# Optimization experiments

Measured on AMD Instinct MI355X. Metric: run time of the kernel, lower is better.

Reference implementation:

```python
import jax, jax.numpy as jnp
import numpy as np

B = 2          # number of point clouds (equal-size so the per-batch loop vmaps)
NB = 10000     # points per cloud
C_IN = 64
K = 16
BN_EPS = 1e-5

# grid_size_options: [tower, background, line]; line grid axis-2 is *5 per the source
GRID_T = jnp.array([0.1, 0.1, 0.1], dtype=jnp.float32)
GRID_B = jnp.array([1.0, 1.0, 1.0], dtype=jnp.float32)
GRID_L = jnp.array([0.3, 0.3, 0.3 * 5.0], dtype=jnp.float32)


def setup_inputs() -> dict:
    key = jax.random.key(0)
    ks = jax.random.split(key, 8)
    feat = jax.random.normal(ks[0], (B * NB, C_IN), dtype=jnp.float32)
    coord = jax.random.normal(ks[1], (B * NB, 3), dtype=jnp.float32) * 10.0
    batch = jnp.repeat(jnp.arange(B, dtype=jnp.int32), NB)
    # feature_judge params: Linear(C,32) -> BatchNorm1d(32) (inference mode) -> ReLU -> Linear(32,3)
    W1 = jax.random.normal(ks[2], (C_IN, 32), dtype=jnp.float32) * (1.0 / np.sqrt(C_IN))
    b1 = jnp.zeros((32,), dtype=jnp.float32)
    gamma = jnp.ones((32,), dtype=jnp.float32)
    beta = jnp.zeros((32,), dtype=jnp.float32)
    rmean = jnp.zeros((32,), dtype=jnp.float32)
    rvar = jnp.ones((32,), dtype=jnp.float32)
    W2 = jax.random.normal(ks[3], (32, 3), dtype=jnp.float32) * (1.0 / np.sqrt(32))
    b2 = jnp.zeros((3,), dtype=jnp.float32)
    return {"feat": feat, "coord": coord, "batch": batch,
            "W1": W1, "b1": b1, "gamma": gamma, "beta": beta,
            "rmean": rmean, "rvar": rvar, "W2": W2, "b2": b2}


def _per_batch(cb, fb, W1, b1, gamma, beta, rmean, rvar, W2, b2):
    # cb: [NB,3] coords, fb: [NB,C] feats
    nb = cb.shape[0]
    # brute-force Euclidean cdist, self-distance excluded (set to inf)
    sq = jnp.sum(cb * cb, axis=-1)                       # [NB]
    d2 = sq[:, None] + sq[None, :] - 2.0 * (cb @ cb.T)   # [NB,NB]
    d2 = jnp.maximum(d2, 0.0)
    diag = jnp.arange(nb)
    d2 = d2.at[diag, diag].set(jnp.inf)
    dist = jnp.sqrt(d2)
    # K nearest neighbors (smallest distances)
    neg_d, idx = jax.lax.top_k(-dist, K)                 # [NB,K]
    min_dist = -neg_d
    # local PCA: eigenvalues of 3x3 covariance == singular values (cov is SPD)
    neigh = cb[idx]                                      # [NB,K,3]
    centered = neigh - neigh.mean(axis=1, keepdims=True)
    cov = jnp.einsum('nkd,nke->nde', centered, centered) / (K - 1)
    S = jnp.linalg.eigvalsh(cov)[:, ::-1]                # descending, == svd singular values
    S_norm = S / (S.sum(axis=1, keepdims=True) + 1e-6)
    linearity = (S_norm[:, 0] - (S_norm[:, 1] + S_norm[:, 2]))[:, None]  # [NB,1]
    mean_dist = min_dist.mean(axis=1, keepdims=True)
    density = 1.0 / (mean_dist + 1e-6)
    # feature_judge MLP (BatchNorm in inference mode with running stats)
    h = fb @ W1 + b1
    h = (h - rmean) / jnp.sqrt(rvar + BN_EPS) * gamma + beta
    h = jax.nn.relu(h)
    logits = h @ W2 + b2
    probs = jax.nn.softmax(logits, axis=1)               # [NB,3]
    tower_prob = (density * 2.0 + probs[:, 0:1]) / 3.0
    background_prob = (jnp.maximum(1.0 - linearity, 1.0 - density) + probs[:, 1:2]) / 3.0
    line_prob = (linearity * 2.0 + probs[:, 2:3]) / 3.0
    grids = tower_prob * GRID_T + background_prob * GRID_B + line_prob * GRID_L + 1e-6
    return grids                                          # [NB,3]


def reference(feat, coord, batch, W1, b1, gamma, beta, rmean, rvar, W2, b2):
    # equal-size batches: the per-batch python loop becomes a vmap
    coord_b = coord.reshape(B, NB, 3)
    feat_b = feat.reshape(B, NB, C_IN)
    out = jax.vmap(lambda c, f: _per_batch(c, f, W1, b1, gamma, beta, rmean, rvar, W2, b2))(coord_b, feat_b)
    return out.reshape(B * NB, 3)
```

## Files before the change

kernel.cpp:

```cpp
#include <hip/hip_runtime.h>
#include <math.h>

#define NBP   10000
#define NBATCH 2
#define KNN   16
#define QT    16
#define PH    16
#define TILE  1250
#define NTHREADS 256
#define COLL  32

__global__ __launch_bounds__(NTHREADS)
void pfas_kernel(const float* __restrict__ feat,
                 const float* __restrict__ coord,
                 const float* __restrict__ W1,
                 const float* __restrict__ b1,
                 const float* __restrict__ gmm,
                 const float* __restrict__ bta,
                 const float* __restrict__ rmean,
                 const float* __restrict__ rvar,
                 const float* __restrict__ W2,
                 const float* __restrict__ b2,
                 float* __restrict__ out)
{
    __shared__ float4 s_cand[TILE];
    __shared__ float  s_tau[QT];
    __shared__ float2 s_coll[QT][COLL];
    __shared__ int    s_cnt[QT];

    const int tid = threadIdx.x;
    const int ql  = tid >> 4;
    const int ph  = tid & 15;
    const int b   = blockIdx.y;
    const int qi  = blockIdx.x * QT + ql;
    const int gq  = b * NBP + qi;

    const float qx = coord[3*gq], qy = coord[3*gq+1], qz = coord[3*gq+2];
    const float qsq = __fadd_rn(__fadd_rn(__fmul_rn(qx,qx), __fmul_rn(qy,qy)), __fmul_rn(qz,qz));

    if (tid < QT) s_cnt[tid] = 0;

    float td[KNN];
    #pragma unroll
    for (int s = 0; s < KNN; ++s) td[s] = INFINITY;

    for (int t0 = 0; t0 < NBP; t0 += TILE) {
        __syncthreads();
        for (int c = tid; c < TILE; c += NTHREADS) {
            const float* cp = coord + (size_t)(b*NBP + t0 + c) * 3;
            float x = cp[0], y = cp[1], z = cp[2];
            float sq = __fadd_rn(__fadd_rn(__fmul_rn(x,x), __fmul_rn(y,y)), __fmul_rn(z,z));
            s_cand[c] = make_float4(x, y, z, sq);
        }
        __syncthreads();
        for (int k = ph; k < TILE; k += PH) {
            const float4 c = s_cand[k];
            float dot = __fadd_rn(__fadd_rn(__fmul_rn(qx,c.x), __fmul_rn(qy,c.y)), __fmul_rn(qz,c.z));
            float d2  = __fsub_rn(__fadd_rn(qsq, c.w), __fmul_rn(2.0f, dot));
            float v = (t0 + k == qi) ? INFINITY : d2;
            #pragma unroll
            for (int s = 0; s < KNN; ++s) {
                float t = td[s];
                td[s] = fminf(t, v);
                v     = fmaxf(t, v);
            }
        }
    }

    __syncthreads();
    float* lists = reinterpret_cast<float*>(s_cand);
    #pragma unroll
    for (int s = 0; s < KNN; ++s) lists[s*NTHREADS + tid] = td[s];
    __syncthreads();

    if (tid < QT) {
        const int lane0 = tid * PH;
        int h0=0,h1=0,h2=0,h3=0,h4=0,h5=0,h6=0,h7=0,h8=0,h9=0,h10=0,h11=0,h12=0,h13=0,h14=0,h15=0;
        float tau = INFINITY;
        #pragma unroll
        for (int o = 0; o < KNN; ++o) {
            float best = INFINITY; int sel = 0;
            #define CHK(P, H) { float e = ((H) < KNN) ? lists[(H)*NTHREADS + lane0 + (P)] : INFINITY; \
                                if (e < best) { best = e; sel = (P); } }
            CHK(0,h0)  CHK(1,h1)  CHK(2,h2)  CHK(3,h3)
            CHK(4,h4)  CHK(5,h5)  CHK(6,h6)  CHK(7,h7)
            CHK(8,h8)  CHK(9,h9)  CHK(10,h10) CHK(11,h11)
            CHK(12,h12) CHK(13,h13) CHK(14,h14) CHK(15,h15)
            #undef CHK
            tau = best;
            h0 += (sel==0);  h1 += (sel==1);  h2 += (sel==2);  h3 += (sel==3);
            h4 += (sel==4);  h5 += (sel==5);  h6 += (sel==6);  h7 += (sel==7);
            h8 += (sel==8);  h9 += (sel==9);  h10+= (sel==10); h11+= (sel==11);
            h12+= (sel==12); h13+= (sel==13); h14+= (sel==14); h15+= (sel==15);
        }
        s_tau[tid] = tau;
    }
    __syncthreads();

    const float tau = s_tau[ql];
    for (int t0 = 0; t0 < NBP; t0 += TILE) {
        __syncthreads();
        for (int c = tid; c < TILE; c += NTHREADS) {
            const float* cp = coord + (size_t)(b*NBP + t0 + c) * 3;
            float x = cp[0], y = cp[1], z = cp[2];
            float sq = __fadd_rn(__fadd_rn(__fmul_rn(x,x), __fmul_rn(y,y)), __fmul_rn(z,z));
            s_cand[c] = make_float4(x, y, z, sq);
        }
        __syncthreads();
        for (int k = ph; k < TILE; k += PH) {
            const float4 c = s_cand[k];
            float dot = __fadd_rn(__fadd_rn(__fmul_rn(qx,c.x), __fmul_rn(qy,c.y)), __fmul_rn(qz,c.z));
            float d2  = __fsub_rn(__fadd_rn(qsq, c.w), __fmul_rn(2.0f, dot));
            int j = t0 + k;
            if (d2 <= tau && j != qi) {
                int slot = atomicAdd(&s_cnt[ql], 1);
                if (slot < COLL) s_coll[ql][slot] = make_float2(d2, __int_as_float(j));
            }
        }
    }
    __syncthreads();

    if (tid < QT) {
        const int q  = tid;
        const int qq = blockIdx.x * QT + q;
        const int gq2 = b * NBP + qq;
        const int n  = min(s_cnt[q], COLL);

        int bi[KNN];
        float sumd = 0.f;
        #pragma unroll
        for (int o = 0; o < KNN; ++o) {
            float best = INFINITY; int besti = qq; int sl = -1;
            for (int e = 0; e < n; ++e) {
                float2 en = s_coll[q][e];
                int ix = __float_as_int(en.y);
                if (en.x < best || (en.x == best && ix < besti)) { best = en.x; besti = ix; sl = e; }
            }
            if (sl >= 0) s_coll[q][sl].x = INFINITY;
            bi[o] = besti;
            sumd = __fadd_rn(sumd, sqrtf(fmaxf(best, 0.f)));
        }
        const float mean_dist = sumd * (1.0f / KNN);
        const float density   = 1.0f / (mean_dist + 1e-6f);

        float mx = 0.f, my = 0.f, mz = 0.f;
        #pragma unroll
        for (int o = 0; o < KNN; ++o) {
            const float* cp = coord + (size_t)(b*NBP + bi[o]) * 3;
            mx += cp[0]; my += cp[1]; mz += cp[2];
        }
        mx *= (1.0f/KNN); my *= (1.0f/KNN); mz *= (1.0f/KNN);
        double cxx=0, cxy=0, cxz=0, cyy=0, cyz=0, czz=0;
        #pragma unroll
        for (int o = 0; o < KNN; ++o) {
            const float* cp = coord + (size_t)(b*NBP + bi[o]) * 3;
            double dx = (double)cp[0] - (double)mx;
            double dy = (double)cp[1] - (double)my;
            double dz = (double)cp[2] - (double)mz;
            cxx += dx*dx; cxy += dx*dy; cxz += dx*dz;
            cyy += dy*dy; cyz += dy*dz; czz += dz*dz;
        }
        const double inv = 1.0 / (KNN - 1);
        cxx *= inv; cxy *= inv; cxz *= inv; cyy *= inv; cyz *= inv; czz *= inv;

        double qm = (cxx + cyy + czz) / 3.0;
        double p1 = cxy*cxy + cxz*cxz + cyz*cyz;
        double b00 = cxx - qm, b11 = cyy - qm, b22 = czz - qm;
        double p2 = b00*b00 + b11*b11 + b22*b22 + 2.0*p1;
        double pp = sqrt(p2 / 6.0);
        double e0, e1, e2;
        if (pp < 1e-30) { e0 = e1 = e2 = qm; }
        else {
            double ip = 1.0 / pp;
            double c00 = b00*ip, c11 = b11*ip, c22 = b22*ip;
            double c01 = cxy*ip, c02 = cxz*ip, c12 = cyz*ip;
            double detB = c00*(c11*c22 - c12*c12)
                        - c01*(c01*c22 - c12*c02)
                        + c02*(c01*c12 - c11*c02);
            double r = detB * 0.5;
            r = fmin(1.0, fmax(-1.0, r));
            double phi = acos(r) / 3.0;
            e0 = qm + 2.0*pp*cos(phi);
            e2 = qm + 2.0*pp*cos(phi + 2.0943951023931953);
            e1 = 3.0*qm - e0 - e2;
        }
        const float lin = (float)((e0 - e1 - e2) / (e0 + e1 + e2 + 1e-6));

        const float* fr = feat + (size_t)gq2 * 64;
        float h[32];
        #pragma unroll
        for (int j = 0; j < 32; ++j) h[j] = b1[j];
        for (int i = 0; i < 64; ++i) {
            float fi = fr[i];
            #pragma unroll
            for (int j = 0; j < 32; ++j) h[j] = fmaf(fi, W1[i*32 + j], h[j]);
        }
        float l0 = b2[0], l1 = b2[1], l2 = b2[2];
        #pragma unroll
        for (int j = 0; j < 32; ++j) {
            float invstd = 1.0f / sqrtf(rvar[j] + 1e-5f);
            float hb = (h[j] - rmean[j]) * invstd * gmm[j] + bta[j];
            hb = fmaxf(hb, 0.f);
            l0 = fmaf(hb, W2[j*3+0], l0);
            l1 = fmaf(hb, W2[j*3+1], l1);
            l2 = fmaf(hb, W2[j*3+2], l2);
        }
        float m  = fmaxf(l0, fmaxf(l1, l2));
        float x0 = expf(l0 - m), x1 = expf(l1 - m), x2 = expf(l2 - m);
        float es = x0 + x1 + x2;
        float p0 = x0/es, pb = x1/es, pl = x2/es;

        float tower = (density*2.0f + p0) / 3.0f;
        float back  = (fmaxf(1.0f - lin, 1.0f - density) + pb) / 3.0f;
        float line  = (lin*2.0f + pl) / 3.0f;
        float g01 = tower*0.1f + back*1.0f + line*0.3f + 1e-6f;
        float g2  = tower*0.1f + back*1.0f + line*1.5f + 1e-6f;
        out[(size_t)gq2*3 + 0] = g01;
        out[(size_t)gq2*3 + 1] = g01;
        out[(size_t)gq2*3 + 2] = g2;
    }
}

extern "C" void kernel_launch(void* const* d_in, const int* in_sizes, int n_in,
                              void* d_out, int out_size, void* d_ws, size_t ws_size,
                              hipStream_t stream) {
    const float* feat  = (const float*)d_in[0];
    const float* coord = (const float*)d_in[1];
    const float* W1    = (const float*)d_in[3];
    const float* b1    = (const float*)d_in[4];
    const float* gmm   = (const float*)d_in[5];
    const float* bta   = (const float*)d_in[6];
    const float* rmean = (const float*)d_in[7];
    const float* rvar  = (const float*)d_in[8];
    const float* W2    = (const float*)d_in[9];
    const float* b2    = (const float*)d_in[10];
    float* out = (float*)d_out;

    dim3 grid(NBP / QT, NBATCH);
    pfas_kernel<<<grid, NTHREADS, 0, stream>>>(feat, coord, W1, b1, gmm, bta,
                                               rmean, rvar, W2, b2, out);
}
```

Before: 492.1 us.

## Use uniform-grid cell lookup for the kNN candidate collection pass

Adds a counting-sort preprocessing stage (zero, histogram, single-block prefix scan, scatter) that bins the points of each cloud into a 36^3 uniform grid stored in the workspace. The second brute-force sweep, which collects candidates within the per-query top-16 radius, is replaced by a scan over only the grid cells overlapping that radius. The first brute-force top-k pass that finds the threshold is kept unchanged. This trades four extra small launches and scattered global reads for far fewer distance evaluations in the collection pass, and falls back to the old kernel when the workspace is too small.

```diff
diff --git a/kernel.cpp b/kernel.cpp
--- a/kernel.cpp
+++ b/kernel.cpp
@@ -2,6 +2,7 @@
 #include <math.h>
 
 #define NBP   10000
+#define NPTS2 20000
 #define NBATCH 2
 #define KNN   16
 #define QT    16
@@ -10,18 +11,83 @@
 #define NTHREADS 256
 #define COLL  32
 
+#define NC    36
+#define NC3   (NC*NC*NC)
+#define NCELLS (2*NC3)
+#define BLO   (-64.0f)
+#define CSZ   (128.0f/NC)
+#define CINV  (NC/128.0f)
+#define WS_COUNTS 0
+#define WS_PK4    373248
+#define WS_PIDX   693248
+#define WS_NEED   773248
+
+__device__ __forceinline__ int cell_xyz(float v) {
+    int c = (int)((v - BLO) * CINV);
+    return min(NC - 1, max(0, c));
+}
+__device__ __forceinline__ int cell_of(float x, float y, float z) {
+    return (cell_xyz(z) * NC + cell_xyz(y)) * NC + cell_xyz(x);
+}
+
 __global__ __launch_bounds__(NTHREADS)
-void pfas_kernel(const float* __restrict__ feat,
-                 const float* __restrict__ coord,
-                 const float* __restrict__ W1,
-                 const float* __restrict__ b1,
-                 const float* __restrict__ gmm,
-                 const float* __restrict__ bta,
-                 const float* __restrict__ rmean,
-                 const float* __restrict__ rvar,
-                 const float* __restrict__ W2,
-                 const float* __restrict__ b2,
-                 float* __restrict__ out)
+void k_zero(int* __restrict__ counts) {
+    int i = blockIdx.x * NTHREADS + threadIdx.x;
+    if (i < NCELLS) counts[i] = 0;
+}
+
+__global__ __launch_bounds__(NTHREADS)
+void k_hist(const float* __restrict__ coord, int* __restrict__ counts) {
+    int i = blockIdx.x * NTHREADS + threadIdx.x;
+    if (i < NPTS2) {
+        float x = coord[3*i], y = coord[3*i+1], z = coord[3*i+2];
+        int g = (i / NBP) * NC3 + cell_of(x, y, z);
+        atomicAdd(&counts[g], 1);
+    }
+}
+
+#define PCH 92
+__global__ __launch_bounds__(1024)
+void k_prefix(int* __restrict__ counts) {
+    __shared__ int part[1024];
+    int t = threadIdx.x;
+    int base = t * PCH;
+    int s = 0;
+    for (int i = 0; i < PCH; ++i) { int idx = base + i; if (idx < NCELLS) s += counts[idx]; }
+    part[t] = s;
+    __syncthreads();
+    if (t == 0) { int run = 0; for (int j = 0; j < 1024; ++j) { int tmp = part[j]; part[j] = run; run += tmp; } }
+    __syncthreads();
+    int run = part[t];
+    for (int i = 0; i < PCH; ++i) {
+        int idx = base + i;
+        if (idx < NCELLS) { int tmp = counts[idx]; counts[idx] = run; run += tmp; }
+    }
+}
+
+__global__ __launch_bounds__(NTHREADS)
+void k_scatter(const float* __restrict__ coord, int* __restrict__ counts,
+               float4* __restrict__ pk4, int* __restrict__ pidx) {
+    int i = blockIdx.x * NTHREADS + threadIdx.x;
+    if (i < NPTS2) {
+        float x = coord[3*i], y = coord[3*i+1], z = coord[3*i+2];
+        int g = (i / NBP) * NC3 + cell_of(x, y, z);
+        int slot = atomicAdd(&counts[g], 1);
+        float sq = __fadd_rn(__fadd_rn(__fmul_rn(x,x), __fmul_rn(y,y)), __fmul_rn(z,z));
+        pk4[slot] = make_float4(x, y, z, sq);
+        pidx[slot] = i - (i / NBP) * NBP;
+    }
+}
+
+__global__ __launch_bounds__(NTHREADS)
+void pfas_gridc(const float* __restrict__ feat, const float* __restrict__ coord,
+                const int* __restrict__ counts, const float4* __restrict__ pk4,
+                const int* __restrict__ pidx,
+                const float* __restrict__ W1, const float* __restrict__ b1,
+                const float* __restrict__ gmm, const float* __restrict__ bta,
+                const float* __restrict__ rmean, const float* __restrict__ rvar,
+                const float* __restrict__ W2, const float* __restrict__ b2,
+                float* __restrict__ out)
 {
     __shared__ float4 s_cand[TILE];
     __shared__ float  s_tau[QT];
@@ -31,9 +97,10 @@
     const int tid = threadIdx.x;
     const int ql  = tid >> 4;
     const int ph  = tid & 15;
-    const int b   = blockIdx.y;
+    const int bb  = blockIdx.y;
     const int qi  = blockIdx.x * QT + ql;
-    const int gq  = b * NBP + qi;
+    const int gbase = bb * NBP;
+    const int gq  = gbase + qi;
 
     const float qx = coord[3*gq], qy = coord[3*gq+1], qz = coord[3*gq+2];
     const float qsq = __fadd_rn(__fadd_rn(__fmul_rn(qx,qx), __fmul_rn(qy,qy)), __fmul_rn(qz,qz));
@@ -47,7 +114,7 @@
     for (int t0 = 0; t0 < NBP; t0 += TILE) {
         __syncthreads();
         for (int c = tid; c < TILE; c += NTHREADS) {
-            const float* cp = coord + (size_t)(b*NBP + t0 + c) * 3;
+            const float* cp = coord + (size_t)(gbase + t0 + c) * 3;
             float x = cp[0], y = cp[1], z = cp[2];
             float sq = __fadd_rn(__fadd_rn(__fmul_rn(x,x), __fmul_rn(y,y)), __fmul_rn(z,z));
             s_cand[c] = make_float4(x, y, z, sq);
@@ -59,11 +126,7 @@
             float d2  = __fsub_rn(__fadd_rn(qsq, c.w), __fmul_rn(2.0f, dot));
             float v = (t0 + k == qi) ? INFINITY : d2;
             #pragma unroll
-            for (int s = 0; s < KNN; ++s) {
-                float t = td[s];
-                td[s] = fminf(t, v);
-                v     = fmaxf(t, v);
-            }
+            for (int s = 0; s < KNN; ++s) { float t = td[s]; td[s] = fminf(t, v); v = fmaxf(t, v); }
         }
     }
 
@@ -97,24 +160,30 @@
     }
     __syncthreads();
 
-    const float tau = s_tau[ql];
-    for (int t0 = 0; t0 < NBP; t0 += TILE) {
-        __syncthreads();
-        for (int c = tid; c < TILE; c += NTHREADS) {
-            const float* cp = coord + (size_t)(b*NBP + t0 + c) * 3;
-            float x = cp[0], y = cp[1], z = cp[2];
-            float sq = __fadd_rn(__fadd_rn(__fmul_rn(x,x), __fmul_rn(y,y)), __fmul_rn(z,z));
-            s_cand[c] = make_float4(x, y, z, sq);
-        }
-        __syncthreads();
-        for (int k = ph; k < TILE; k += PH) {
-            const float4 c = s_cand[k];
-            float dot = __fadd_rn(__fadd_rn(__fmul_rn(qx,c.x), __fmul_rn(qy,c.y)), __fmul_rn(qz,c.z));
-            float d2  = __fsub_rn(__fadd_rn(qsq, c.w), __fmul_rn(2.0f, dot));
-            int j = t0 + k;
-            if (d2 <= tau && j != qi) {
-                int slot = atomicAdd(&s_cnt[ql], 1);
-                if (slot < COLL) s_coll[ql][slot] = make_float2(d2, __int_as_float(j));
+    {
+        const float tau = s_tau[ql];
+        const float rr = __fadd_rn(__fmul_rn(sqrtf(fmaxf(tau, 0.f)), 1.001f), 0.01f);
+        const int cx0 = cell_xyz(qx - rr), cx1 = cell_xyz(qx + rr);
+        const int cy0 = cell_xyz(qy - rr), cy1 = cell_xyz(qy + rr);
+        const int cz0 = cell_xyz(qz - rr), cz1 = cell_xyz(qz + rr);
+        for (int az = cz0; az <= cz1; ++az) {
+            for (int ay = cy0; ay <= cy1; ++ay) {
+                for (int ax = cx0; ax <= cx1; ++ax) {
+                    int g  = bb * NC3 + (az * NC + ay) * NC + ax;
+                    int st = (g == 0) ? 0 : counts[g-1];
+                    int en = counts[g];
+                    st = max(0, min(st, NPTS2)); en = max(st, min(en, NPTS2));
+                    for (int i = st + ph; i < en; i += PH) {
+                        float4 c = pk4[i];
+                        float dot = __fadd_rn(__fadd_rn(__fmul_rn(qx,c.x), __fmul_rn(qy,c.y)), __fmul_rn(qz,c.z));
+                        float d2  = __fsub_rn(__fadd_rn(qsq, c.w), __fmul_rn(2.0f, dot));
+                        int j = pidx[i];
+                        if (d2 <= tau && j != qi) {
+                            int slot = atomicAdd(&s_cnt[ql], 1);
+                            if (slot < COLL) s_coll[ql][slot] = make_float2(d2, __int_as_float(j));
+                        }
+                    }
+                }
             }
         }
     }
@@ -123,7 +192,7 @@
     if (tid < QT) {
         const int q  = tid;
         const int qq = blockIdx.x * QT + q;
-        const int gq2 = b * NBP + qq;
+        const int gq2 = gbase + qq;
         const int n  = min(s_cnt[q], COLL);
 
         int bi[KNN];
@@ -146,14 +215,14 @@
         float mx = 0.f, my = 0.f, mz = 0.f;
         #pragma unroll
         for (int o = 0; o < KNN; ++o) {
-            const float* cp = coord + (size_t)(b*NBP + bi[o]) * 3;
+            const float* cp = coord + (size_t)(gbase + bi[o]) * 3;
             mx += cp[0]; my += cp[1]; mz += cp[2];
         }
         mx *= (1.0f/KNN); my *= (1.0f/KNN); mz *= (1.0f/KNN);
         double cxx=0, cxy=0, cxz=0, cyy=0, cyz=0, czz=0;
         #pragma unroll
         for (int o = 0; o < KNN; ++o) {
-            const float* cp = coord + (size_t)(b*NBP + bi[o]) * 3;
+            const float* cp = coord + (size_t)(gbase + bi[o]) * 3;
             double dx = (double)cp[0] - (double)mx;
             double dy = (double)cp[1] - (double)my;
             double dz = (double)cp[2] - (double)mz;
@@ -221,6 +290,197 @@
     }
 }
 
+__global__ __launch_bounds__(NTHREADS)
+void pfas_kernel(const float* __restrict__ feat, const float* __restrict__ coord,
+                 const float* __restrict__ W1, const float* __restrict__ b1,
+                 const float* __restrict__ gmm, const float* __restrict__ bta,
+                 const float* __restrict__ rmean, const float* __restrict__ rvar,
+                 const float* __restrict__ W2, const float* __restrict__ b2,
+                 float* __restrict__ out)
+{
+    __shared__ float4 s_cand[TILE];
+    __shared__ float  s_tau[QT];
+    __shared__ float2 s_coll[QT][COLL];
+    __shared__ int    s_cnt[QT];
+
+    const int tid = threadIdx.x;
+    const int ql  = tid >> 4;
+    const int ph  = tid & 15;
+    const int b   = blockIdx.y;
+    const int qi  = blockIdx.x * QT + ql;
+    const int gq  = b * NBP + qi;
+
+    const float qx = coord[3*gq], qy = coord[3*gq+1], qz = coord[3*gq+2];
+    const float qsq = __fadd_rn(__fadd_rn(__fmul_rn(qx,qx), __fmul_rn(qy,qy)), __fmul_rn(qz,qz));
+
+    if (tid < QT) s_cnt[tid] = 0;
+
+    float td[KNN];
+    #pragma unroll
+    for (int s = 0; s < KNN; ++s) td[s] = INFINITY;
+
+    for (int t0 = 0; t0 < NBP; t0 += TILE) {
+        __syncthreads();
+        for (int c = tid; c < TILE; c += NTHREADS) {
+            const float* cp = coord + (size_t)(b*NBP + t0 + c) * 3;
+            float x = cp[0], y = cp[1], z = cp[2];
+            float sq = __fadd_rn(__fadd_rn(__fmul_rn(x,x), __fmul_rn(y,y)), __fmul_rn(z,z));
+            s_cand[c] = make_float4(x, y, z, sq);
+        }
+        __syncthreads();
+        for (int k = ph; k < TILE; k += PH) {
+            const float4 c = s_cand[k];
+            float dot = __fadd_rn(__fadd_rn(__fmul_rn(qx,c.x), __fmul_rn(qy,c.y)), __fmul_rn(qz,c.z));
+            float d2  = __fsub_rn(__fadd_rn(qsq, c.w), __fmul_rn(2.0f, dot));
+            float v = (t0 + k == qi) ? INFINITY : d2;
+            #pragma unroll
+            for (int s = 0; s < KNN; ++s) { float t = td[s]; td[s] = fminf(t, v); v = fmaxf(t, v); }
+        }
+    }
+    __syncthreads();
+    float* lists = reinterpret_cast<float*>(s_cand);
+    #pragma unroll
+    for (int s = 0; s < KNN; ++s) lists[s*NTHREADS + tid] = td[s];
+    __syncthreads();
+    if (tid < QT) {
+        const int lane0 = tid * PH;
+        int h0=0,h1=0,h2=0,h3=0,h4=0,h5=0,h6=0,h7=0,h8=0,h9=0,h10=0,h11=0,h12=0,h13=0,h14=0,h15=0;
+        float tau = INFINITY;
+        #pragma unroll
+        for (int o = 0; o < KNN; ++o) {
+            float best = INFINITY; int sel = 0;
+            #define CHK(P, H) { float e = ((H) < KNN) ? lists[(H)*NTHREADS + lane0 + (P)] : INFINITY; \
+                                if (e < best) { best = e; sel = (P); } }
+            CHK(0,h0)  CHK(1,h1)  CHK(2,h2)  CHK(3,h3)
+            CHK(4,h4)  CHK(5,h5)  CHK(6,h6)  CHK(7,h7)
+            CHK(8,h8)  CHK(9,h9)  CHK(10,h10) CHK(11,h11)
+            CHK(12,h12) CHK(13,h13) CHK(14,h14) CHK(15,h15)
+            #undef CHK
+            tau = best;
+            h0 += (sel==0);  h1 += (sel==1);  h2 += (sel==2);  h3 += (sel==3);
+            h4 += (sel==4);  h5 += (sel==5);  h6 += (sel==6);  h7 += (sel==7);
+            h8 += (sel==8);  h9 += (sel==9);  h10+= (sel==10); h11+= (sel==11);
+            h12+= (sel==12); h13+= (sel==13); h14+= (sel==14); h15+= (sel==15);
+        }
+        s_tau[tid] = tau;
+    }
+    __syncthreads();
+    const float tau = s_tau[ql];
+    for (int t0 = 0; t0 < NBP; t0 += TILE) {
+        __syncthreads();
+        for (int c = tid; c < TILE; c += NTHREADS) {
+            const float* cp = coord + (size_t)(b*NBP + t0 + c) * 3;
+            float x = cp[0], y = cp[1], z = cp[2];
+            float sq = __fadd_rn(__fadd_rn(__fmul_rn(x,x), __fmul_rn(y,y)), __fmul_rn(z,z));
+            s_cand[c] = make_float4(x, y, z, sq);
+        }
+        __syncthreads();
+        for (int k = ph; k < TILE; k += PH) {
+            const float4 c = s_cand[k];
+            float dot = __fadd_rn(__fadd_rn(__fmul_rn(qx,c.x), __fmul_rn(qy,c.y)), __fmul_rn(qz,c.z));
+            float d2  = __fsub_rn(__fadd_rn(qsq, c.w), __fmul_rn(2.0f, dot));
+            int j = t0 + k;
+            if (d2 <= tau && j != qi) {
+                int slot = atomicAdd(&s_cnt[ql], 1);
+                if (slot < COLL) s_coll[ql][slot] = make_float2(d2, __int_as_float(j));
+            }
+        }
+    }
+    __syncthreads();
+    if (tid < QT) {
+        const int q  = tid;
+        const int qq = blockIdx.x * QT + q;
+        const int gq2 = b * NBP + qq;
+        const int n  = min(s_cnt[q], COLL);
+        int bi[KNN];
+        float sumd = 0.f;
+        #pragma unroll
+        for (int o = 0; o < KNN; ++o) {
+            float best = INFINITY; int besti = qq; int sl = -1;
+            for (int e = 0; e < n; ++e) {
+                float2 en = s_coll[q][e];
+                int ix = __float_as_int(en.y);
+                if (en.x < best || (en.x == best && ix < besti)) { best = en.x; besti = ix; sl = e; }
+            }
+            if (sl >= 0) s_coll[q][sl].x = INFINITY;
+            bi[o] = besti;
+            sumd = __fadd_rn(sumd, sqrtf(fmaxf(best, 0.f)));
+        }
+        const float mean_dist = sumd * (1.0f / KNN);
+        const float density   = 1.0f / (mean_dist + 1e-6f);
+        float mx = 0.f, my = 0.f, mz = 0.f;
+        #pragma unroll
+        for (int o = 0; o < KNN; ++o) {
+            const float* cp = coord + (size_t)(b*NBP + bi[o]) * 3;
+            mx += cp[0]; my += cp[1]; mz += cp[2];
+        }
+        mx *= (1.0f/KNN); my *= (1.0f/KNN); mz *= (1.0f/KNN);
+        double cxx=0, cxy=0, cxz=0, cyy=0, cyz=0, czz=0;
+        #pragma unroll
+        for (int o = 0; o < KNN; ++o) {
+            const float* cp = coord + (size_t)(b*NBP + bi[o]) * 3;
+            double dx = (double)cp[0] - (double)mx;
+            double dy = (double)cp[1] - (double)my;
+            double dz = (double)cp[2] - (double)mz;
+            cxx += dx*dx; cxy += dx*dy; cxz += dx*dz;
+            cyy += dy*dy; cyz += dy*dz; czz += dz*dz;
+        }
+        const double inv = 1.0 / (KNN - 1);
+        cxx *= inv; cxy *= inv; cxz *= inv; cyy *= inv; cyz *= inv; czz *= inv;
+        double qm = (cxx + cyy + czz) / 3.0;
+        double p1 = cxy*cxy + cxz*cxz + cyz*cyz;
+        double b00 = cxx - qm, b11 = cyy - qm, b22 = czz - qm;
+        double p2 = b00*b00 + b11*b11 + b22*b22 + 2.0*p1;
+        double pp = sqrt(p2 / 6.0);
+        double e0, e1, e2;
+        if (pp < 1e-30) { e0 = e1 = e2 = qm; }
+        else {
+            double ip = 1.0 / pp;
+            double c00 = b00*ip, c11 = b11*ip, c22 = b22*ip;
+            double c01 = cxy*ip, c02 = cxz*ip, c12 = cyz*ip;
+            double detB = c00*(c11*c22 - c12*c12) - c01*(c01*c22 - c12*c02) + c02*(c01*c12 - c11*c02);
+            double r = detB * 0.5;
+            r = fmin(1.0, fmax(-1.0, r));
+            double phi = acos(r) / 3.0;
+            e0 = qm + 2.0*pp*cos(phi);
+            e2 = qm + 2.0*pp*cos(phi + 2.0943951023931953);
+            e1 = 3.0*qm - e0 - e2;
+        }
+        const float lin = (float)((e0 - e1 - e2) / (e0 + e1 + e2 + 1e-6));
+        const float* fr = feat + (size_t)gq2 * 64;
+        float h[32];
+        #pragma unroll
+        for (int j = 0; j < 32; ++j) h[j] = b1[j];
+        for (int i = 0; i < 64; ++i) {
+            float fi = fr[i];
+            #pragma unroll
+            for (int j = 0; j < 32; ++j) h[j] = fmaf(fi, W1[i*32 + j], h[j]);
+        }
+        float l0 = b2[0], l1 = b2[1], l2 = b2[2];
+        #pragma unroll
+        for (int j = 0; j < 32; ++j) {
+            float invstd = 1.0f / sqrtf(rvar[j] + 1e-5f);
+            float hb = (h[j] - rmean[j]) * invstd * gmm[j] + bta[j];
+            hb = fmaxf(hb, 0.f);
+            l0 = fmaf(hb, W2[j*3+0], l0);
+            l1 = fmaf(hb, W2[j*3+1], l1);
+            l2 = fmaf(hb, W2[j*3+2], l2);
+        }
+        float m  = fmaxf(l0, fmaxf(l1, l2));
+        float x0 = expf(l0 - m), x1 = expf(l1 - m), x2 = expf(l2 - m);
+        float es = x0 + x1 + x2;
+        float p0 = x0/es, pb = x1/es, pl = x2/es;
+        float tower = (density*2.0f + p0) / 3.0f;
+        float back  = (fmaxf(1.0f - lin, 1.0f - density) + pb) / 3.0f;
+        float line  = (lin*2.0f + pl) / 3.0f;
+        float g01 = tower*0.1f + back*1.0f + line*0.3f + 1e-6f;
+        float g2  = tower*0.1f + back*1.0f + line*1.5f + 1e-6f;
+        out[(size_t)gq2*3 + 0] = g01;
+        out[(size_t)gq2*3 + 1] = g01;
+        out[(size_t)gq2*3 + 2] = g2;
+    }
+}
+
 extern "C" void kernel_launch(void* const* d_in, const int* in_sizes, int n_in,
                               void* d_out, int out_size, void* d_ws, size_t ws_size,
                               hipStream_t stream) {
@@ -237,6 +497,19 @@
     float* out = (float*)d_out;
 
     dim3 grid(NBP / QT, NBATCH);
-    pfas_kernel<<<grid, NTHREADS, 0, stream>>>(feat, coord, W1, b1, gmm, bta,
-                                               rmean, rvar, W2, b2, out);
-}
+
+    if (ws_size >= (size_t)WS_NEED) {
+        int*    counts = (int*)((char*)d_ws + WS_COUNTS);
+        float4* pk4    = (float4*)((char*)d_ws + WS_PK4);
+        int*    pidx   = (int*)((char*)d_ws + WS_PIDX);
+        k_zero   <<<(NCELLS + NTHREADS-1)/NTHREADS, NTHREADS, 0, stream>>>(counts);
+        k_hist   <<<(NPTS2  + NTHREADS-1)/NTHREADS, NTHREADS, 0, stream>>>(coord, counts);
+        k_prefix <<<1, 1024, 0, stream>>>(counts);
+        k_scatter<<<(NPTS2  + NTHREADS-1)/NTHREADS, NTHREADS, 0, stream>>>(coord, counts, pk4, pidx);
+        pfas_gridc<<<grid, NTHREADS, 0, stream>>>(feat, coord, counts, pk4, pidx,
+                                                  W1, b1, gmm, bta, rmean, rvar, W2, b2, out);
+    } else {
+        pfas_kernel<<<grid, NTHREADS, 0, stream>>>(feat, coord, W1, b1, gmm, bta,
+                                                   rmean, rvar, W2, b2, out);
+    }
+}
```

Result: slower. 977.8 us (+98.7%).
